# Performance work log

Measured on AMD Instinct MI355X. Metric: run time of the kernel, lower is better.

Reference implementation:

```python
import jax, jax.numpy as jnp
import numpy as np

B, L, E, H = 4, 2048, 512, 8
HD = E // H
EPS = 1e-6


def setup_inputs() -> dict:
    key = jax.random.key(0)
    ks = jax.random.split(key, 9)
    s = 0.02
    return {
        "query": jax.random.normal(ks[0], (B, L, E), dtype=jnp.float32),
        "Wq": jax.random.normal(ks[1], (E, E), dtype=jnp.float32) * s,
        "bq": jnp.zeros((E,), dtype=jnp.float32),
        "Wk": jax.random.normal(ks[2], (E, E), dtype=jnp.float32) * s,
        "bk": jnp.zeros((E,), dtype=jnp.float32),
        "Wv": jax.random.normal(ks[3], (E, E), dtype=jnp.float32) * s,
        "bv": jnp.zeros((E,), dtype=jnp.float32),
        "Wo": jax.random.normal(ks[4], (E, E), dtype=jnp.float32) * s,
        "bo": jnp.zeros((E,), dtype=jnp.float32),
    }


def reference(query, Wq, bq, Wk, bk, Wv, bv, Wo, bo):
    b, tgt_len, embed_dim = query.shape
    n_head = H
    head_dim = embed_dim // n_head
    # Faithful to the source: a raw view (reshape), NOT a transpose.
    x = query.reshape(tgt_len, b, embed_dim)  # (L, B, E)
    q = x @ Wq.T + bq
    k = x @ Wk.T + bk
    v = x @ Wv.T + bv
    # softmax over head_dim, per head
    q = jax.nn.softmax(q.reshape(tgt_len, b, n_head, head_dim), axis=-1)
    k = jax.nn.softmax(k.reshape(tgt_len, b, n_head, head_dim), axis=-1)
    # (L, B*H, hd) -> (B*H, L, hd)
    q_ = q.reshape(tgt_len, b * n_head, head_dim).swapaxes(0, 1)
    k_ = k.reshape(tgt_len, b * n_head, head_dim).swapaxes(0, 1)
    comp_q_ = 1.0 - q_
    comp_k_ = 1.0 - k_
    v_ = v.reshape(tgt_len, b * n_head, head_dim).swapaxes(0, 1)
    # non-causal XNor attention: scores from q.k^T + (1-q).(1-k)^T
    weights = jnp.einsum('nld,nsd->nls', q_, k_) + jnp.einsum('nld,nsd->nls', comp_q_, comp_k_)
    denom = jnp.clip(jnp.sum(weights, axis=-1, keepdims=True), EPS, None)
    attn_weights = weights / denom
    attn_output = jnp.einsum('nls,nsd->nld', attn_weights, v_)  # (B*H, L, hd)
    attn_output = attn_output.swapaxes(0, 1).reshape(tgt_len, b, embed_dim)
    out = attn_output @ Wo.T + bo
    return out.reshape(b, tgt_len, embed_dim)
```

## Files before the change

### kernel.cpp

```cpp
#include <hip/hip_runtime.h>

#define B_ 4
#define L_ 2048
#define E_ 512
#define H_ 8
#define NROW (B_*L_)
#define SZ (NROW*E_)
#define NH (B_*H_)

typedef unsigned short u16;
typedef unsigned int u32;
typedef __attribute__((ext_vector_type(8))) __bf16 bf16x8;
typedef __attribute__((ext_vector_type(8))) u16 u16x8;
typedef __attribute__((ext_vector_type(4))) float f32x4;

__device__ __forceinline__ u16 f2bf(float f) {
  union { float f; u32 u; } v; v.f = f;
  u32 r = v.u + 0x7FFFu + ((v.u >> 16) & 1u);
  return (u16)(r >> 16);
}
__device__ __forceinline__ float bf2f(u16 s) {
  union { u32 u; float f; } v; v.u = ((u32)s) << 16;
  return v.f;
}
__device__ __forceinline__ void async16(const u16* g, u16* l) {
  __builtin_amdgcn_global_load_lds(
      (const __attribute__((address_space(1))) u32*)g,
      (__attribute__((address_space(3))) u32*)l, 16, 0, 0);
}

__global__ __launch_bounds__(256) void cvt_all(const float* __restrict__ X,
    const float* __restrict__ W0, const float* __restrict__ W1,
    const float* __restrict__ W2, const float* __restrict__ W3,
    u16* __restrict__ Y, u16* __restrict__ Y0, u16* __restrict__ Y1,
    u16* __restrict__ Y2, u16* __restrict__ Y3) {
  const int bid = blockIdx.x;
  const float* src;
  u16* dst;
  int off;
  if (bid < 2048) { src = X; dst = Y; off = bid * 2048; }
  else {
    const int t = bid - 2048, s = t >> 7, r = t & 127;
    src = (s == 0) ? W0 : (s == 1) ? W1 : (s == 2) ? W2 : W3;
    dst = (s == 0) ? Y0 : (s == 1) ? Y1 : (s == 2) ? Y2 : Y3;
    off = r * 2048;
  }
  const int i0 = off + threadIdx.x * 8;
  f32x4 a = *(const f32x4*)(src + i0);
  f32x4 b = *(const f32x4*)(src + i0 + 4);
  u16x8 o;
#pragma unroll
  for (int j = 0; j < 4; ++j) { o[j] = f2bf(a[j]); o[4 + j] = f2bf(b[j]); }
  *(u16x8*)(dst + i0) = o;
}

__global__ __launch_bounds__(256, 3) void qkv_gemm(const u16* __restrict__ X,
    const u16* __restrict__ Wq, const u16* __restrict__ Wk, const u16* __restrict__ Wv,
    const float* __restrict__ bq, const float* __restrict__ bk, const float* __restrict__ bv,
    u16* __restrict__ Qo, u16* __restrict__ Ko, u16* __restrict__ Vo) {
  __shared__ __align__(16) union {
    struct { u16 a[2][128 * 32]; u16 b[2][128 * 32]; } st;
    u16 ep[4][16 * 72];
  } sh;
  const int z = blockIdx.z;
  const u16* W = (z == 0) ? Wq : (z == 1) ? Wk : Wv;
  const float* bias = (z == 0) ? bq : (z == 1) ? bk : bv;
  u16* C = (z == 0) ? Qo : (z == 1) ? Ko : Vo;
  const int tid = threadIdx.x;
  const int w = tid >> 6, lane = tid & 63;
  const int bm = blockIdx.x * 128, bn = blockIdx.y * 128;
  const int wm = (w >> 1) * 64, wn = (w & 1) * 64;
  const int fr = lane & 15, quad = lane >> 4;
  const int c0 = tid, c1 = tid + 256;
  const int ar0 = c0 >> 2, ak0 = (c0 & 3) * 8;
  const int ar1 = c1 >> 2, ak1 = (c1 & 3) * 8;
  f32x4 acc[4][4] = {};
  for (int k0 = 0; k0 < E_; k0 += 64) {
    __syncthreads();
#pragma unroll
    for (int p = 0; p < 2; ++p) {
      const int kp = k0 + p * 32;
      async16(X + (size_t)(bm + ar0) * E_ + kp + ak0, sh.st.a[p] + c0 * 8);
      async16(X + (size_t)(bm + ar1) * E_ + kp + ak1, sh.st.a[p] + c1 * 8);
      async16(W + (size_t)(bn + ar0) * E_ + kp + ak0, sh.st.b[p] + c0 * 8);
      async16(W + (size_t)(bn + ar1) * E_ + kp + ak1, sh.st.b[p] + c1 * 8);
    }
    __syncthreads();
#pragma unroll
    for (int p = 0; p < 2; ++p) {
      bf16x8 af[4], bf[4];
#pragma unroll
      for (int t = 0; t < 4; ++t) {
        af[t] = *(const bf16x8*)(sh.st.a[p] + (wm + t * 16 + fr) * 32 + quad * 8);
        bf[t] = *(const bf16x8*)(sh.st.b[p] + (wn + t * 16 + fr) * 32 + quad * 8);
      }
#pragma unroll
      for (int i = 0; i < 4; ++i)
#pragma unroll
        for (int j = 0; j < 4; ++j)
          acc[i][j] = __builtin_amdgcn_mfma_f32_16x16x32_bf16(af[i], bf[j], acc[i][j], 0, 0, 0);
    }
  }
  __syncthreads();
  u16* ep = sh.ep[w];
#pragma unroll
  for (int i = 0; i < 4; ++i) {
    if (z < 2) {
#pragma unroll
      for (int r = 0; r < 4; ++r) {
        float v[4];
#pragma unroll
        for (int nt = 0; nt < 4; ++nt)
          v[nt] = acc[i][nt][r] + bias[bn + wn + nt * 16 + fr];
        float e[4], ssum = 0.f;
#pragma unroll
        for (int nt = 0; nt < 4; ++nt) { e[nt] = __expf(v[nt]); ssum += e[nt]; }
#pragma unroll
        for (int off = 1; off < 16; off <<= 1) ssum += __shfl_xor(ssum, off, 64);
        const float inv = 1.f / ssum;
#pragma unroll
        for (int nt = 0; nt < 4; ++nt)
          ep[(quad * 4 + r) * 72 + nt * 16 + fr] = f2bf(e[nt] * inv);
      }
    } else {
#pragma unroll
      for (int r = 0; r < 4; ++r)
#pragma unroll
        for (int nt = 0; nt < 4; ++nt)
          ep[(quad * 4 + r) * 72 + nt * 16 + fr] =
              f2bf(acc[i][nt][r] + bias[bn + wn + nt * 16 + fr]);
    }
#pragma unroll
    for (int pass = 0; pass < 2; ++pass) {
      const int row = pass * 8 + (lane >> 3), ch = lane & 7;
      u16x8 val = *(const u16x8*)(ep + row * 72 + ch * 8);
      *(u16x8*)(C + (size_t)(bm + wm + i * 16 + row) * E_ + bn + wn + ch * 8) = val;
    }
  }
}

__global__ __launch_bounds__(256) void gemm_out(const u16* __restrict__ X,
    const u16* __restrict__ W, const float* __restrict__ bias, float* __restrict__ C) {
  __shared__ __align__(16) union {
    struct { u16 a[2][128 * 32]; u16 b[2][64 * 32]; } st;
    float ep[4][16 * 68];
  } sh;
  const int tid = threadIdx.x;
  const int w = tid >> 6, lane = tid & 63;
  const int bm = blockIdx.x * 128, bn = blockIdx.y * 64;
  const int fr = lane & 15, quad = lane >> 4;
  const int c0 = tid, c1 = tid + 256;
  const int ar0 = c0 >> 2, ak0 = (c0 & 3) * 8;
  const int ar1 = c1 >> 2, ak1 = (c1 & 3) * 8;
  f32x4 acc[2][4] = {};
  for (int k0 = 0; k0 < E_; k0 += 64) {
    __syncthreads();
#pragma unroll
    for (int p = 0; p < 2; ++p) {
      const int kp = k0 + p * 32;
      async16(X + (size_t)(bm + ar0) * E_ + kp + ak0, sh.st.a[p] + c0 * 8);
      async16(X + (size_t)(bm + ar1) * E_ + kp + ak1, sh.st.a[p] + c1 * 8);
      async16(W + (size_t)(bn + ar0) * E_ + kp + ak0, sh.st.b[p] + c0 * 8);
    }
    __syncthreads();
#pragma unroll
    for (int p = 0; p < 2; ++p) {
      bf16x8 af[2], bf[4];
#pragma unroll
      for (int mt = 0; mt < 2; ++mt)
        af[mt] = *(const bf16x8*)(sh.st.a[p] + (w * 32 + mt * 16 + fr) * 32 + quad * 8);
#pragma unroll
      for (int nt = 0; nt < 4; ++nt)
        bf[nt] = *(const bf16x8*)(sh.st.b[p] + (nt * 16 + fr) * 32 + quad * 8);
#pragma unroll
      for (int mt = 0; mt < 2; ++mt)
#pragma unroll
        for (int nt = 0; nt < 4; ++nt)
          acc[mt][nt] = __builtin_amdgcn_mfma_f32_16x16x32_bf16(af[mt], bf[nt],
                                                                acc[mt][nt], 0, 0, 0);
    }
  }
  __syncthreads();
  float* ep = sh.ep[w];
#pragma unroll
  for (int mt = 0; mt < 2; ++mt) {
#pragma unroll
    for (int r = 0; r < 4; ++r)
#pragma unroll
      for (int nt = 0; nt < 4; ++nt)
        ep[(quad * 4 + r) * 68 + nt * 16 + fr] = acc[mt][nt][r] + bias[bn + nt * 16 + fr];
#pragma unroll
    for (int p = 0; p < 4; ++p) {
      const int id = p * 64 + lane;
      const int row = id >> 4, ch = id & 15;
      f32x4 val = *(const f32x4*)(ep + row * 68 + ch * 4);
      *(f32x4*)(C + (size_t)(bm + w * 32 + mt * 16 + row) * E_ + bn + ch * 4) = val;
    }
  }
}

__global__ __launch_bounds__(256) void kv_part(const u16* __restrict__ K,
    const u16* __restrict__ V, float* __restrict__ Part,
    float* __restrict__ KPart, float* __restrict__ VPart) {
  __shared__ __align__(16) union {
    u16 stg[4][2][2][64 * 40];
    float red[3][64][100];
  } sh;
  const int n = blockIdx.x, b = n >> 3, h = n & 7;
  const int sy = blockIdx.y;
  const int tid = threadIdx.x, w = tid >> 6, lane = tid & 63;
  const int lr = lane >> 1, half = lane & 1;
  const int fr = lane & 15, quad = lane >> 4;
  const int e0 = half * 32;
  const int row0 = sy * 512 + w * 128;
  f32x4 acc[4][4] = {};
  f32x4 accK[4] = {};
  f32x4 accV[4] = {};
  union { u16x8 u; bf16x8 b; } one;
#pragma unroll
  for (int j = 0; j < 8; ++j) one.u[j] = 0x3F80;
  u16x8 rK[4], rV[4], nK[4], nV[4];
  {
    const u16* gK = K + (size_t)((row0 + lr) * B_ + b) * E_ + h * 64 + e0;
    const u16* gV = V + (size_t)((row0 + lr) * B_ + b) * E_ + h * 64 + e0;
#pragma unroll
    for (int q = 0; q < 4; ++q) {
      rK[q] = *(const u16x8*)(gK + q * 8);
      rV[q] = *(const u16x8*)(gV + q * 8);
    }
  }
#pragma unroll
  for (int c = 0; c < 4; ++c) {
    const int buf = c & 1;
    u16* dK = &sh.stg[w][buf][0][0];
    u16* dV = &sh.stg[w][buf][1][0];
#pragma unroll
    for (int q = 0; q < 4; ++q)
#pragma unroll
      for (int j = 0; j < 8; ++j) {
        const int e = e0 + q * 8 + j;
        dK[e * 40 + lr] = rK[q][j];
        dV[e * 40 + lr] = rV[q][j];
      }
    if (c < 3) {
      const u16* gK = K + (size_t)((row0 + (c + 1) * 32 + lr) * B_ + b) * E_ + h * 64 + e0;
      const u16* gV = V + (size_t)((row0 + (c + 1) * 32 + lr) * B_ + b) * E_ + h * 64 + e0;
#pragma unroll
      for (int q = 0; q < 4; ++q) {
        nK[q] = *(const u16x8*)(gK + q * 8);
        nV[q] = *(const u16x8*)(gV + q * 8);
      }
    }
    bf16x8 af[4], bf[4];
#pragma unroll
    for (int t = 0; t < 4; ++t) {
      af[t] = *(const bf16x8*)(dV + (t * 16 + fr) * 40 + quad * 8);
      bf[t] = *(const bf16x8*)(dK + (t * 16 + fr) * 40 + quad * 8);
    }
#pragma unroll
    for (int i = 0; i < 4; ++i)
#pragma unroll
      for (int j = 0; j < 4; ++j)
        acc[i][j] = __builtin_amdgcn_mfma_f32_16x16x32_bf16(af[i], bf[j], acc[i][j], 0, 0, 0);
#pragma unroll
    for (int j = 0; j < 4; ++j)
      accK[j] = __builtin_amdgcn_mfma_f32_16x16x32_bf16(one.b, bf[j], accK[j], 0, 0, 0);
#pragma unroll
    for (int i = 0; i < 4; ++i)
      accV[i] = __builtin_amdgcn_mfma_f32_16x16x32_bf16(af[i], one.b, accV[i], 0, 0, 0);
#pragma unroll
    for (int q = 0; q < 4; ++q) { rK[q] = nK[q]; rV[q] = nV[q]; }
  }
  __syncthreads();
  if (w > 0) {
    float* rp = &sh.red[w - 1][lane][0];
#pragma unroll
    for (int t = 0; t < 16; ++t) *(f32x4*)(rp + t * 4) = acc[t >> 2][t & 3];
#pragma unroll
    for (int t = 0; t < 4; ++t) *(f32x4*)(rp + 64 + t * 4) = accK[t];
#pragma unroll
    for (int t = 0; t < 4; ++t) *(f32x4*)(rp + 80 + t * 4) = accV[t];
  }
  __syncthreads();
  if (w == 0) {
#pragma unroll
    for (int p = 0; p < 3; ++p) {
      const float* rp = &sh.red[p][lane][0];
#pragma unroll
      for (int t = 0; t < 16; ++t) acc[t >> 2][t & 3] += *(const f32x4*)(rp + t * 4);
#pragma unroll
      for (int t = 0; t < 4; ++t) accK[t] += *(const f32x4*)(rp + 64 + t * 4);
#pragma unroll
      for (int t = 0; t < 4; ++t) accV[t] += *(const f32x4*)(rp + 80 + t * 4);
    }
    float* Pp = Part + (size_t)(n * 4 + sy) * 4096;
#pragma unroll
    for (int i = 0; i < 4; ++i)
#pragma unroll
      for (int j = 0; j < 4; ++j)
#pragma unroll
        for (int r = 0; r < 4; ++r)
          Pp[(i * 16 + quad * 4 + r) * 64 + j * 16 + fr] = acc[i][j][r];
    if (quad == 0) {
#pragma unroll
      for (int j = 0; j < 4; ++j)
        KPart[(n * 4 + sy) * 64 + j * 16 + fr] = accK[j][0];
    }
    if (fr == 0) {
#pragma unroll
      for (int i = 0; i < 4; ++i)
#pragma unroll
        for (int r = 0; r < 4; ++r)
          VPart[(n * 4 + sy) * 64 + i * 16 + quad * 4 + r] = accV[i][r];
    }
  }
}

__global__ __launch_bounds__(256) void apply_mfma(const u16* __restrict__ Qbf,
    const float* __restrict__ Part, const float* __restrict__ KPart,
    const float* __restrict__ VPart, u16* __restrict__ Abf) {
  __shared__ __align__(16) u16 sQ[128 * 64];
  __shared__ __align__(16) u16 sM[64 * 64];
  __shared__ float sKs[64], sVs[64], sDen[128];
  const int n = blockIdx.x, b = n >> 3, h = n & 7;
  const int l0 = blockIdx.y * 128;
  const int tid = threadIdx.x, w = tid >> 6, lane = tid & 63;
  const int fr = lane & 15, quad = lane >> 4;
#pragma unroll
  for (int j = 0; j < 4; ++j) {
    const int rloc = w * 32 + j * 8;
    const int row = rloc + (lane >> 3);
    const int k = (lane & 7) * 8;
    async16(Qbf + (size_t)((l0 + row) * B_ + b) * E_ + h * 64 + k, sQ + rloc * 64);
  }
  {
    const int e = tid >> 2, d0 = (tid & 3) * 16;
    const float* Pp = Part + (size_t)n * 4 * 4096 + e * 64 + d0;
    f32x4 s0 = {}, s1 = {}, s2 = {}, s3 = {};
#pragma unroll
    for (int s = 0; s < 4; ++s) {
      const float* q = Pp + s * 4096;
      s0 += *(const f32x4*)(q);
      s1 += *(const f32x4*)(q + 4);
      s2 += *(const f32x4*)(q + 8);
      s3 += *(const f32x4*)(q + 12);
    }
    u16x8 o0, o1;
#pragma unroll
    for (int j = 0; j < 4; ++j) {
      o0[j] = f2bf(s0[j]); o0[4 + j] = f2bf(s1[j]);
      o1[j] = f2bf(s2[j]); o1[4 + j] = f2bf(s3[j]);
    }
    *(u16x8*)(sM + e * 64 + d0) = o0;
    *(u16x8*)(sM + e * 64 + d0 + 8) = o1;
  }
  if (tid < 64) {
    float s = 0.f;
#pragma unroll
    for (int sl = 0; sl < 4; ++sl) s += KPart[(n * 4 + sl) * 64 + tid];
    sKs[tid] = s;
  } else if (tid < 128) {
    float s = 0.f;
#pragma unroll
    for (int sl = 0; sl < 4; ++sl) s += VPart[(n * 4 + sl) * 64 + tid - 64];
    sVs[tid - 64] = s;
  }
  __syncthreads();
  union { u16x8 u; bf16x8 bv; } aU[2][2];
  bf16x8 bF[4][2];
#pragma unroll
  for (int mt = 0; mt < 2; ++mt)
#pragma unroll
    for (int ks = 0; ks < 2; ++ks)
      aU[mt][ks].u = *(const u16x8*)(sQ + (w * 32 + mt * 16 + fr) * 64 + ks * 32 + quad * 8);
#pragma unroll
  for (int nt = 0; nt < 4; ++nt)
#pragma unroll
    for (int ks = 0; ks < 2; ++ks)
      bF[nt][ks] = *(const bf16x8*)(sM + (nt * 16 + fr) * 64 + ks * 32 + quad * 8);
  float pden[2] = {0.f, 0.f};
#pragma unroll
  for (int mt = 0; mt < 2; ++mt)
#pragma unroll
    for (int ks = 0; ks < 2; ++ks)
#pragma unroll
      for (int j = 0; j < 8; ++j)
        pden[mt] = fmaf(bf2f(aU[mt][ks].u[j]), sKs[ks * 32 + quad * 8 + j], pden[mt]);
#pragma unroll
  for (int mt = 0; mt < 2; ++mt) {
    pden[mt] += __shfl_xor(pden[mt], 16, 64);
    pden[mt] += __shfl_xor(pden[mt], 32, 64);
    if (quad == 0)
      sDen[w * 32 + mt * 16 + fr] = fmaxf(2.f * pden[mt] + 62.f * (float)L_, 1e-6f);
  }
  __syncthreads();
  f32x4 acc[2][4];
#pragma unroll
  for (int mt = 0; mt < 2; ++mt)
#pragma unroll
    for (int nt = 0; nt < 4; ++nt) {
      const float iv = 31.f * sVs[nt * 16 + fr];
      acc[mt][nt] = (f32x4){iv, iv, iv, iv};
#pragma unroll
      for (int ks = 0; ks < 2; ++ks)
        acc[mt][nt] = __builtin_amdgcn_mfma_f32_16x16x32_bf16(aU[mt][ks].bv, bF[nt][ks],
                                                              acc[mt][nt], 0, 0, 0);
    }
#pragma unroll
  for (int mt = 0; mt < 2; ++mt)
#pragma unroll
    for (int r = 0; r < 4; ++r) {
      const int rloc = w * 32 + mt * 16 + quad * 4 + r;
      const float invd = 2.f / sDen[rloc];
      const size_t orow = (size_t)((l0 + rloc) * B_ + b) * E_ + h * 64;
#pragma unroll
      for (int nt = 0; nt < 4; ++nt)
        Abf[orow + nt * 16 + fr] = f2bf(acc[mt][nt][r] * invd);
    }
}

extern "C" void kernel_launch(void* const* d_in, const int* in_sizes, int n_in,
                              void* d_out, int out_size, void* d_ws, size_t ws_size,
                              hipStream_t stream) {
  const float* query = (const float*)d_in[0];
  const float* Wq = (const float*)d_in[1];
  const float* bq = (const float*)d_in[2];
  const float* Wk = (const float*)d_in[3];
  const float* bk = (const float*)d_in[4];
  const float* Wv = (const float*)d_in[5];
  const float* bv = (const float*)d_in[6];
  const float* Wo = (const float*)d_in[7];
  const float* bo = (const float*)d_in[8];
  float* out = (float*)d_out;

  char* ws = (char*)d_ws;
  u16* Xbf  = (u16*)(ws);
  u16* Qbf  = (u16*)(ws + 8388608);
  u16* Kbf  = (u16*)(ws + 16777216);
  u16* Vbf  = (u16*)(ws + 25165824);
  u16* Abf  = (u16*)(ws + 33554432);
  u16* Wqb  = (u16*)(ws + 41943040);
  u16* Wkb  = (u16*)(ws + 42467328);
  u16* Wvb  = (u16*)(ws + 42991616);
  u16* Wob  = (u16*)(ws + 43515904);
  float* KPart = (float*)(ws + 44580864);
  float* VPart = (float*)(ws + 44711936);
  float* Part  = (float*)Xbf;

  cvt_all<<<2560, 256, 0, stream>>>(query, Wq, Wk, Wv, Wo,
                                    Xbf, Wqb, Wkb, Wvb, Wob);
  qkv_gemm<<<dim3(NROW / 128, E_ / 128, 3), 256, 0, stream>>>(
      Xbf, Wqb, Wkb, Wvb, bq, bk, bv, Qbf, Kbf, Vbf);
  kv_part<<<dim3(NH, 4), 256, 0, stream>>>(Kbf, Vbf, Part, KPart, VPart);
  apply_mfma<<<dim3(NH, L_ / 128), 256, 0, stream>>>(Qbf, Part, KPart, VPart, Abf);
  gemm_out<<<dim3(NROW / 128, E_ / 64), 256, 0, stream>>>(Abf, Wob, bo, out);
}
```

Before: 129.3 us.

## Fuse Q/K/V projections per block and split KV reduction into more slices

qkv_gemm now computes all three projections in one block for a 128x64 output tile. Each X tile is staged in shared memory once and reused against the Wq, Wk and Wv tiles, instead of being reloaded by three separate z-blocks. Occupancy is lowered to 2 blocks per SM because of the larger accumulator set. kv_part now splits the sequence into 8 slices instead of 4, doubling its grid to fill more CUs. In exchange, apply_mfma sums twice as many partial results.

Result: slower. 133.9 us (+3.5%).

```diff
diff --git a/kernel.cpp b/kernel.cpp
--- a/kernel.cpp
+++ b/kernel.cpp
@@ -54,27 +54,23 @@
   *(u16x8*)(dst + i0) = o;
 }
 
-__global__ __launch_bounds__(256, 3) void qkv_gemm(const u16* __restrict__ X,
+__global__ __launch_bounds__(256, 2) void qkv_gemm(const u16* __restrict__ X,
     const u16* __restrict__ Wq, const u16* __restrict__ Wk, const u16* __restrict__ Wv,
     const float* __restrict__ bq, const float* __restrict__ bk, const float* __restrict__ bv,
     u16* __restrict__ Qo, u16* __restrict__ Ko, u16* __restrict__ Vo) {
   __shared__ __align__(16) union {
-    struct { u16 a[2][128 * 32]; u16 b[2][128 * 32]; } st;
+    struct { u16 a[2][128 * 32]; u16 b[3][2][64 * 32]; } st;
     u16 ep[4][16 * 72];
   } sh;
-  const int z = blockIdx.z;
-  const u16* W = (z == 0) ? Wq : (z == 1) ? Wk : Wv;
-  const float* bias = (z == 0) ? bq : (z == 1) ? bk : bv;
-  u16* C = (z == 0) ? Qo : (z == 1) ? Ko : Vo;
   const int tid = threadIdx.x;
   const int w = tid >> 6, lane = tid & 63;
-  const int bm = blockIdx.x * 128, bn = blockIdx.y * 128;
-  const int wm = (w >> 1) * 64, wn = (w & 1) * 64;
+  const int bm = blockIdx.x * 128, bn = blockIdx.y * 64;
   const int fr = lane & 15, quad = lane >> 4;
   const int c0 = tid, c1 = tid + 256;
   const int ar0 = c0 >> 2, ak0 = (c0 & 3) * 8;
   const int ar1 = c1 >> 2, ak1 = (c1 & 3) * 8;
-  f32x4 acc[4][4] = {};
+  const int wr = tid >> 2, wk = (tid & 3) * 8;
+  f32x4 acc[3][2][4] = {};
   for (int k0 = 0; k0 < E_; k0 += 64) {
     __syncthreads();
 #pragma unroll
@@ -82,59 +78,71 @@
       const int kp = k0 + p * 32;
       async16(X + (size_t)(bm + ar0) * E_ + kp + ak0, sh.st.a[p] + c0 * 8);
       async16(X + (size_t)(bm + ar1) * E_ + kp + ak1, sh.st.a[p] + c1 * 8);
-      async16(W + (size_t)(bn + ar0) * E_ + kp + ak0, sh.st.b[p] + c0 * 8);
-      async16(W + (size_t)(bn + ar1) * E_ + kp + ak1, sh.st.b[p] + c1 * 8);
+      async16(Wq + (size_t)(bn + wr) * E_ + kp + wk, sh.st.b[0][p] + tid * 8);
+      async16(Wk + (size_t)(bn + wr) * E_ + kp + wk, sh.st.b[1][p] + tid * 8);
+      async16(Wv + (size_t)(bn + wr) * E_ + kp + wk, sh.st.b[2][p] + tid * 8);
     }
     __syncthreads();
 #pragma unroll
     for (int p = 0; p < 2; ++p) {
-      bf16x8 af[4], bf[4];
-#pragma unroll
-      for (int t = 0; t < 4; ++t) {
-        af[t] = *(const bf16x8*)(sh.st.a[p] + (wm + t * 16 + fr) * 32 + quad * 8);
-        bf[t] = *(const bf16x8*)(sh.st.b[p] + (wn + t * 16 + fr) * 32 + quad * 8);
+      bf16x8 af[2];
+#pragma unroll
+      for (int mt = 0; mt < 2; ++mt)
+        af[mt] = *(const bf16x8*)(sh.st.a[p] + (w * 32 + mt * 16 + fr) * 32 + quad * 8);
+#pragma unroll
+      for (int z = 0; z < 3; ++z) {
+        bf16x8 bf[4];
+#pragma unroll
+        for (int nt = 0; nt < 4; ++nt)
+          bf[nt] = *(const bf16x8*)(sh.st.b[z][p] + (nt * 16 + fr) * 32 + quad * 8);
+#pragma unroll
+        for (int mt = 0; mt < 2; ++mt)
+#pragma unroll
+          for (int nt = 0; nt < 4; ++nt)
+            acc[z][mt][nt] = __builtin_amdgcn_mfma_f32_16x16x32_bf16(af[mt], bf[nt],
+                                                                     acc[z][mt][nt], 0, 0, 0);
       }
-#pragma unroll
-      for (int i = 0; i < 4; ++i)
-#pragma unroll
-        for (int j = 0; j < 4; ++j)
-          acc[i][j] = __builtin_amdgcn_mfma_f32_16x16x32_bf16(af[i], bf[j], acc[i][j], 0, 0, 0);
     }
   }
   __syncthreads();
   u16* ep = sh.ep[w];
 #pragma unroll
-  for (int i = 0; i < 4; ++i) {
-    if (z < 2) {
-#pragma unroll
-      for (int r = 0; r < 4; ++r) {
-        float v[4];
-#pragma unroll
-        for (int nt = 0; nt < 4; ++nt)
-          v[nt] = acc[i][nt][r] + bias[bn + wn + nt * 16 + fr];
-        float e[4], ssum = 0.f;
-#pragma unroll
-        for (int nt = 0; nt < 4; ++nt) { e[nt] = __expf(v[nt]); ssum += e[nt]; }
-#pragma unroll
-        for (int off = 1; off < 16; off <<= 1) ssum += __shfl_xor(ssum, off, 64);
-        const float inv = 1.f / ssum;
-#pragma unroll
-        for (int nt = 0; nt < 4; ++nt)
-          ep[(quad * 4 + r) * 72 + nt * 16 + fr] = f2bf(e[nt] * inv);
+  for (int z = 0; z < 3; ++z) {
+    u16* C = (z == 0) ? Qo : (z == 1) ? Ko : Vo;
+    const float* bias = (z == 0) ? bq : (z == 1) ? bk : bv;
+#pragma unroll
+    for (int mt = 0; mt < 2; ++mt) {
+      if (z < 2) {
+#pragma unroll
+        for (int r = 0; r < 4; ++r) {
+          float v[4];
+#pragma unroll
+          for (int nt = 0; nt < 4; ++nt)
+            v[nt] = acc[z][mt][nt][r] + bias[bn + nt * 16 + fr];
+          float e[4], ssum = 0.f;
+#pragma unroll
+          for (int nt = 0; nt < 4; ++nt) { e[nt] = __expf(v[nt]); ssum += e[nt]; }
+#pragma unroll
+          for (int off = 1; off < 16; off <<= 1) ssum += __shfl_xor(ssum, off, 64);
+          const float inv = 1.f / ssum;
+#pragma unroll
+          for (int nt = 0; nt < 4; ++nt)
+            ep[(quad * 4 + r) * 72 + nt * 16 + fr] = f2bf(e[nt] * inv);
+        }
+      } else {
+#pragma unroll
+        for (int r = 0; r < 4; ++r)
+#pragma unroll
+          for (int nt = 0; nt < 4; ++nt)
+            ep[(quad * 4 + r) * 72 + nt * 16 + fr] =
+                f2bf(acc[z][mt][nt][r] + bias[bn + nt * 16 + fr]);
       }
-    } else {
-#pragma unroll
-      for (int r = 0; r < 4; ++r)
-#pragma unroll
-        for (int nt = 0; nt < 4; ++nt)
-          ep[(quad * 4 + r) * 72 + nt * 16 + fr] =
-              f2bf(acc[i][nt][r] + bias[bn + wn + nt * 16 + fr]);
-    }
-#pragma unroll
-    for (int pass = 0; pass < 2; ++pass) {
-      const int row = pass * 8 + (lane >> 3), ch = lane & 7;
-      u16x8 val = *(const u16x8*)(ep + row * 72 + ch * 8);
-      *(u16x8*)(C + (size_t)(bm + wm + i * 16 + row) * E_ + bn + wn + ch * 8) = val;
+#pragma unroll
+      for (int pass = 0; pass < 2; ++pass) {
+        const int row = pass * 8 + (lane >> 3), ch = lane & 7;
+        u16x8 val = *(const u16x8*)(ep + row * 72 + ch * 8);
+        *(u16x8*)(C + (size_t)(bm + w * 32 + mt * 16 + row) * E_ + bn + ch * 8) = val;
+      }
     }
   }
 }
@@ -212,7 +220,7 @@
   const int lr = lane >> 1, half = lane & 1;
   const int fr = lane & 15, quad = lane >> 4;
   const int e0 = half * 32;
-  const int row0 = sy * 512 + w * 128;
+  const int row0 = sy * 256 + w * 64;
   f32x4 acc[4][4] = {};
   f32x4 accK[4] = {};
   f32x4 accV[4] = {};
@@ -230,7 +238,7 @@
     }
   }
 #pragma unroll
-  for (int c = 0; c < 4; ++c) {
+  for (int c = 0; c < 2; ++c) {
     const int buf = c & 1;
     u16* dK = &sh.stg[w][buf][0][0];
     u16* dV = &sh.stg[w][buf][1][0];
@@ -242,9 +250,9 @@
         dK[e * 40 + lr] = rK[q][j];
         dV[e * 40 + lr] = rV[q][j];
       }
-    if (c < 3) {
-      const u16* gK = K + (size_t)((row0 + (c + 1) * 32 + lr) * B_ + b) * E_ + h * 64 + e0;
-      const u16* gV = V + (size_t)((row0 + (c + 1) * 32 + lr) * B_ + b) * E_ + h * 64 + e0;
+    if (c < 1) {
+      const u16* gK = K + (size_t)((row0 + 32 + lr) * B_ + b) * E_ + h * 64 + e0;
+      const u16* gV = V + (size_t)((row0 + 32 + lr) * B_ + b) * E_ + h * 64 + e0;
 #pragma unroll
       for (int q = 0; q < 4; ++q) {
         nK[q] = *(const u16x8*)(gK + q * 8);
@@ -293,7 +301,7 @@
 #pragma unroll
       for (int t = 0; t < 4; ++t) accV[t] += *(const f32x4*)(rp + 80 + t * 4);
     }
-    float* Pp = Part + (size_t)(n * 4 + sy) * 4096;
+    float* Pp = Part + (size_t)(n * 8 + sy) * 4096;
 #pragma unroll
     for (int i = 0; i < 4; ++i)
 #pragma unroll
@@ -304,14 +312,14 @@
     if (quad == 0) {
 #pragma unroll
       for (int j = 0; j < 4; ++j)
-        KPart[(n * 4 + sy) * 64 + j * 16 + fr] = accK[j][0];
+        KPart[(n * 8 + sy) * 64 + j * 16 + fr] = accK[j][0];
     }
     if (fr == 0) {
 #pragma unroll
       for (int i = 0; i < 4; ++i)
 #pragma unroll
         for (int r = 0; r < 4; ++r)
-          VPart[(n * 4 + sy) * 64 + i * 16 + quad * 4 + r] = accV[i][r];
+          VPart[(n * 8 + sy) * 64 + i * 16 + quad * 4 + r] = accV[i][r];
     }
   }
 }
@@ -335,10 +343,10 @@
   }
   {
     const int e = tid >> 2, d0 = (tid & 3) * 16;
-    const float* Pp = Part + (size_t)n * 4 * 4096 + e * 64 + d0;
+    const float* Pp = Part + (size_t)n * 8 * 4096 + e * 64 + d0;
     f32x4 s0 = {}, s1 = {}, s2 = {}, s3 = {};
 #pragma unroll
-    for (int s = 0; s < 4; ++s) {
+    for (int s = 0; s < 8; ++s) {
       const float* q = Pp + s * 4096;
       s0 += *(const f32x4*)(q);
       s1 += *(const f32x4*)(q + 4);
@@ -357,12 +365,12 @@
   if (tid < 64) {
     float s = 0.f;
 #pragma unroll
-    for (int sl = 0; sl < 4; ++sl) s += KPart[(n * 4 + sl) * 64 + tid];
+    for (int sl = 0; sl < 8; ++sl) s += KPart[(n * 8 + sl) * 64 + tid];
     sKs[tid] = s;
   } else if (tid < 128) {
     float s = 0.f;
 #pragma unroll
-    for (int sl = 0; sl < 4; ++sl) s += VPart[(n * 4 + sl) * 64 + tid - 64];
+    for (int sl = 0; sl < 8; ++sl) s += VPart[(n * 8 + sl) * 64 + tid - 64];
     sVs[tid - 64] = s;
   }
   __syncthreads();
@@ -449,9 +457,9 @@
 
   cvt_all<<<2560, 256, 0, stream>>>(query, Wq, Wk, Wv, Wo,
                                     Xbf, Wqb, Wkb, Wvb, Wob);
-  qkv_gemm<<<dim3(NROW / 128, E_ / 128, 3), 256, 0, stream>>>(
+  qkv_gemm<<<dim3(NROW / 128, E_ / 64), 256, 0, stream>>>(
       Xbf, Wqb, Wkb, Wvb, bq, bk, bv, Qbf, Kbf, Vbf);
-  kv_part<<<dim3(NH, 4), 256, 0, stream>>>(Kbf, Vbf, Part, KPart, VPart);
+  kv_part<<<dim3(NH, 8), 256, 0, stream>>>(Kbf, Vbf, Part, KPart, VPart);
   apply_mfma<<<dim3(NH, L_ / 128), 256, 0, stream>>>(Qbf, Part, KPart, VPart, Abf);
   gemm_out<<<dim3(NROW / 128, E_ / 64), 256, 0, stream>>>(Abf, Wob, bo, out);
 }
```

## Stage full W tile once in LDS and stream A fragments from registers in gemm_out

Applied to the files above, without the earlier changes.

The output-projection GEMM now loads its entire 64xE slice of Wo into padded shared memory once, instead of double-buffering A and B tiles every 64-wide k step with two barriers per step. Each wave reads its A fragments straight from global memory into registers, prefetching two k-steps ahead. This removes the per-iteration synchronisation and LDS traffic for A. In exchange it uses much more shared memory, which can lower occupancy, and relies on uncoalesced per-lane global loads for A. The added barrier in the epilogue loop looks meant to guard reuse of the ep buffer, which shares the union with the W tile.

Result: slower. 131.9 us (+2.0%).

```diff
diff --git a/kernel.cpp b/kernel.cpp
--- a/kernel.cpp
+++ b/kernel.cpp
@@ -142,43 +142,42 @@
 __global__ __launch_bounds__(256) void gemm_out(const u16* __restrict__ X,
     const u16* __restrict__ W, const float* __restrict__ bias, float* __restrict__ C) {
   __shared__ __align__(16) union {
-    struct { u16 a[2][128 * 32]; u16 b[2][64 * 32]; } st;
+    u16 b[64 * 520];
     float ep[4][16 * 68];
   } sh;
   const int tid = threadIdx.x;
   const int w = tid >> 6, lane = tid & 63;
   const int bm = blockIdx.x * 128, bn = blockIdx.y * 64;
   const int fr = lane & 15, quad = lane >> 4;
-  const int c0 = tid, c1 = tid + 256;
-  const int ar0 = c0 >> 2, ak0 = (c0 & 3) * 8;
-  const int ar1 = c1 >> 2, ak1 = (c1 & 3) * 8;
+#pragma unroll
+  for (int r0 = 0; r0 < 16; ++r0) {
+    const int r = w * 16 + r0;
+    async16(W + (size_t)(bn + r) * E_ + lane * 8, sh.b + r * 520 + lane * 8);
+  }
+  const u16* A0 = X + (size_t)(bm + w * 32 + fr) * E_ + quad * 8;
+  const u16* A1 = X + (size_t)(bm + w * 32 + 16 + fr) * E_ + quad * 8;
+  u16x8 a0a = *(const u16x8*)(A0);       u16x8 a1a = *(const u16x8*)(A1);
+  u16x8 a0b = *(const u16x8*)(A0 + 32);  u16x8 a1b = *(const u16x8*)(A1 + 32);
+  __syncthreads();
   f32x4 acc[2][4] = {};
-  for (int k0 = 0; k0 < E_; k0 += 64) {
-    __syncthreads();
-#pragma unroll
-    for (int p = 0; p < 2; ++p) {
-      const int kp = k0 + p * 32;
-      async16(X + (size_t)(bm + ar0) * E_ + kp + ak0, sh.st.a[p] + c0 * 8);
-      async16(X + (size_t)(bm + ar1) * E_ + kp + ak1, sh.st.a[p] + c1 * 8);
-      async16(W + (size_t)(bn + ar0) * E_ + kp + ak0, sh.st.b[p] + c0 * 8);
-    }
-    __syncthreads();
-#pragma unroll
-    for (int p = 0; p < 2; ++p) {
-      bf16x8 af[2], bf[4];
-#pragma unroll
-      for (int mt = 0; mt < 2; ++mt)
-        af[mt] = *(const bf16x8*)(sh.st.a[p] + (w * 32 + mt * 16 + fr) * 32 + quad * 8);
-#pragma unroll
-      for (int nt = 0; nt < 4; ++nt)
-        bf[nt] = *(const bf16x8*)(sh.st.b[p] + (nt * 16 + fr) * 32 + quad * 8);
-#pragma unroll
-      for (int mt = 0; mt < 2; ++mt)
-#pragma unroll
-        for (int nt = 0; nt < 4; ++nt)
-          acc[mt][nt] = __builtin_amdgcn_mfma_f32_16x16x32_bf16(af[mt], bf[nt],
-                                                                acc[mt][nt], 0, 0, 0);
-    }
+  for (int kp = 0; kp < E_; kp += 32) {
+    u16x8 n0 = a0b, n1 = a1b;
+    if (kp + 64 < E_) {
+      n0 = *(const u16x8*)(A0 + kp + 64);
+      n1 = *(const u16x8*)(A1 + kp + 64);
+    }
+    bf16x8 bf[4];
+#pragma unroll
+    for (int nt = 0; nt < 4; ++nt)
+      bf[nt] = *(const bf16x8*)(sh.b + (nt * 16 + fr) * 520 + kp + quad * 8);
+    union { u16x8 u; bf16x8 b; } af0, af1;
+    af0.u = a0a; af1.u = a1a;
+#pragma unroll
+    for (int nt = 0; nt < 4; ++nt) {
+      acc[0][nt] = __builtin_amdgcn_mfma_f32_16x16x32_bf16(af0.b, bf[nt], acc[0][nt], 0, 0, 0);
+      acc[1][nt] = __builtin_amdgcn_mfma_f32_16x16x32_bf16(af1.b, bf[nt], acc[1][nt], 0, 0, 0);
+    }
+    a0a = a0b; a1a = a1b; a0b = n0; a1b = n1;
   }
   __syncthreads();
   float* ep = sh.ep[w];
@@ -196,6 +195,7 @@
       f32x4 val = *(const f32x4*)(ep + row * 68 + ch * 4);
       *(f32x4*)(C + (size_t)(bm + w * 32 + mt * 16 + row) * E_ + bn + ch * 4) = val;
     }
+    __syncthreads();
   }
 }
 
```
